# Kernel optimization log

Hardware: AMD Instinct MI355X
Metric: run time of the kernel (lower is better)

The kernel has to match this reference:

```python
import jax, jax.numpy as jnp
import numpy as np

HEADS = 16
HEAD_DIM = 64
DIM = 1024
INNER = HEADS * HEAD_DIM
EPS = 1e-5


def setup_inputs() -> dict:
    key = jax.random.key(0)
    ks = jax.random.split(key, 7)
    s_qkv = (2.0 / (DIM + 3 * INNER)) ** 0.5
    s_out = (2.0 / (INNER + DIM)) ** 0.5
    return {
        "x": jax.random.normal(ks[0], (4, 2048, DIM), dtype=jnp.float32),
        "w_qkv": jax.random.normal(ks[1], (DIM, 3 * INNER), dtype=jnp.float32) * s_qkv,
        "b_qkv": jnp.zeros((3 * INNER,), dtype=jnp.float32),
        "w_out": jax.random.normal(ks[2], (INNER, DIM), dtype=jnp.float32) * s_out,
        "b_out": jnp.zeros((DIM,), dtype=jnp.float32),
        "ln_gamma": jnp.ones((DIM,), dtype=jnp.float32),
        "ln_beta": jnp.zeros((DIM,), dtype=jnp.float32),
    }


def reference(x, w_qkv, b_qkv, w_out, b_out, ln_gamma, ln_beta):
    # Pre-norm LayerNorm
    mu = jnp.mean(x, axis=-1, keepdims=True)
    var = jnp.var(x, axis=-1, keepdims=True)
    xn = (x - mu) * jax.lax.rsqrt(var + EPS) * ln_gamma + ln_beta
    # QKV projection: [b, l, 3*inner]
    qkv = xn @ w_qkv + b_qkv
    q, k, v = jnp.split(qkv, 3, axis=-1)
    b, l, _ = x.shape
    def heads(t):  # [b, l, inner] -> [b, h, l, d]
        return t.reshape(b, l, HEADS, HEAD_DIM).transpose(0, 2, 1, 3)
    q, k, v = heads(q), heads(k), heads(v)
    scale = HEAD_DIM ** -0.5
    scores = jnp.einsum('bhqd,bhkd->bhqk', q, k) * scale
    att = jax.nn.softmax(scores, axis=-1)
    out = jnp.einsum('bhqk,bhkd->bhqd', att, v)
    out = out.transpose(0, 2, 1, 3).reshape(b, l, INNER)
    return out @ w_out + b_out
```

## Files before the change

### kernel.cpp

```cpp
#include <hip/hip_runtime.h>
#include <stdint.h>

typedef __bf16 bf16;
typedef bf16 bf16x4 __attribute__((ext_vector_type(4)));
typedef bf16 bf16x8 __attribute__((ext_vector_type(8)));
typedef float f32x4 __attribute__((ext_vector_type(4)));


__device__ __forceinline__ void gll16(const bf16* g, const bf16* l) {
  __builtin_amdgcn_global_load_lds(
      (__attribute__((address_space(1))) void*)(g),
      (__attribute__((address_space(3))) void*)(l),
      16, 0, 0);
}

__global__ __launch_bounds__(256) void ln_kernel(
    const float* __restrict__ x, const float* __restrict__ gamma,
    const float* __restrict__ beta, bf16* __restrict__ xn)
{
  __shared__ float red[8];
  const long row = blockIdx.x;
  const int t = threadIdx.x;
  f32x4 f = *(const f32x4*)(x + row * 1024 + t * 4);
  float sum = f[0] + f[1] + f[2] + f[3];
  float sq  = f[0]*f[0] + f[1]*f[1] + f[2]*f[2] + f[3]*f[3];
#pragma unroll
  for (int sh = 1; sh < 64; sh <<= 1) {
    sum += __shfl_xor(sum, sh, 64);
    sq  += __shfl_xor(sq,  sh, 64);
  }
  const int wave = t >> 6, lane = t & 63;
  if (lane == 0) { red[wave] = sum; red[wave + 4] = sq; }
  __syncthreads();
  sum = red[0] + red[1] + red[2] + red[3];
  sq  = red[4] + red[5] + red[6] + red[7];
  const float mu  = sum * (1.0f / 1024.0f);
  const float var = sq * (1.0f / 1024.0f) - mu * mu;
  const float rs  = rsqrtf(var + 1e-5f);
  f32x4 g = *(const f32x4*)(gamma + t * 4);
  f32x4 bb = *(const f32x4*)(beta + t * 4);
  bf16x4 ov;
#pragma unroll
  for (int i = 0; i < 4; i++)
    ov[i] = (bf16)((f[i] - mu) * rs * g[i] + bb[i]);
  *(bf16x4*)(xn + row * 1024 + t * 4) = ov;
}

__global__ __launch_bounds__(256) void transpose2_kernel(
    const float* __restrict__ wqkv, bf16* __restrict__ wqkvT,
    const float* __restrict__ wout, bf16* __restrict__ woutT)
{
  __shared__ bf16 tile[32][33];
  const int bx = blockIdx.x;
  const float* in;
  bf16* out;
  int Cc, c0;
  if (bx < 96) { in = wqkv; out = wqkvT; Cc = 3072; c0 = bx * 32; }
  else         { in = wout; out = woutT; Cc = 1024; c0 = (bx - 96) * 32; }
  const int r0 = blockIdx.y * 32;
  const int tx = threadIdx.x & 31, ty = threadIdx.x >> 5;
#pragma unroll
  for (int i = 0; i < 32; i += 8)
    tile[ty + i][tx] = (bf16)in[(long)(r0 + ty + i) * Cc + c0 + tx];
  __syncthreads();
#pragma unroll
  for (int i = 0; i < 32; i += 8)
    out[(long)(c0 + ty + i) * 1024 + r0 + tx] = tile[tx][ty + i];
}

__global__ __launch_bounds__(256, 2) void gemm_bt(
    const bf16* __restrict__ A, const bf16* __restrict__ BT,
    const float* __restrict__ bias, float* __restrict__ C,
    bf16* __restrict__ qb, bf16* __restrict__ kb, bf16* __restrict__ vtb,
    int K, int N, int mode)
{
  __shared__ bf16 sA[2][128 * 32];
  __shared__ bf16 sB[2][128 * 32];
  const int t = threadIdx.x;
  const int lane = t & 63;
  const int wave = t >> 6;
  const int wave_u = __builtin_amdgcn_readfirstlane(wave);
  const int quad = lane >> 4;
  const int c16 = lane & 15;
  const int wm = (wave >> 1) * 64;
  const int wn = (wave & 1) * 64;
  const int m0 = blockIdx.x * 128;
  const int n0 = blockIdx.y * 128;

  f32x4 acc[4][4] = {};

  const int srow = t >> 2;
  const int scol = (t & 3) * 8;
  const bf16* gA = A + (long)(m0 + srow) * K + scol;
  const bf16* gB = BT + (long)(n0 + srow) * K + scol;
  const bf16* lA = sA[0] + wave_u * 512;
  const bf16* lB = sB[0] + wave_u * 512;
  const long rowskip = (long)64 * K;

  gll16(gA, lA);
  gll16(gA + rowskip, lA + 2048);
  gll16(gB, lB);
  gll16(gB + rowskip, lB + 2048);

  int cur = 0;
  for (int k0 = 0; k0 < K; k0 += 32) {
    __syncthreads();
    const int kn = k0 + 32;
    if (kn < K) {
      const int alt = cur ^ 1;
      gll16(gA + kn, lA + alt * 4096);
      gll16(gA + kn + rowskip, lA + alt * 4096 + 2048);
      gll16(gB + kn, lB + alt * 4096);
      gll16(gB + kn + rowskip, lB + alt * 4096 + 2048);
    }
    const bf16* cA = sA[0] + cur * 4096;
    const bf16* cB = sB[0] + cur * 4096;
    bf16x8 af[4], bfr[4];
#pragma unroll
    for (int i = 0; i < 4; i++)
      af[i] = *(const bf16x8*)(cA + (wm + i * 16 + c16) * 32 + quad * 8);
#pragma unroll
    for (int j = 0; j < 4; j++)
      bfr[j] = *(const bf16x8*)(cB + (wn + j * 16 + c16) * 32 + quad * 8);
#pragma unroll
    for (int i = 0; i < 4; i++)
#pragma unroll
      for (int j = 0; j < 4; j++)
        acc[i][j] = __builtin_amdgcn_mfma_f32_16x16x32_bf16(af[i], bfr[j], acc[i][j], 0, 0, 0);
    cur ^= 1;
  }

#pragma unroll
  for (int i = 0; i < 4; i++) {
    const int mbase = m0 + wm + i * 16 + quad * 4;
#pragma unroll
    for (int j = 0; j < 4; j++) {
      const int n = n0 + wn + j * 16 + c16;
      const float bv = bias[n];
      if (mode == 0) {
#pragma unroll
        for (int r = 0; r < 4; r++)
          C[(long)(mbase + r) * N + n] = acc[i][j][r] + bv;
      } else {
        const int part = n >> 10;
        const int inner = n & 1023;
        const int h = inner >> 6, d = inner & 63;
#pragma unroll
        for (int r = 0; r < 4; r++) {
          const int m = mbase + r;
          const int b = m >> 11, l = m & 2047;
          const long bh = (long)((b << 4) | h);
          const float v = acc[i][j][r] + bv;
          if (part == 0)      qb [(bh * 2048 + l) * 64 + d] = (bf16)(v * 0.18033688f);
          else if (part == 1) kb [(bh * 2048 + l) * 64 + d] = (bf16)v;
          else                vtb[(bh * 64 + d) * 2048 + l] = (bf16)v;
        }
      }
    }
  }
}

__global__ __launch_bounds__(256, 4) void attn_kernel(
    const bf16* __restrict__ q, const bf16* __restrict__ k,
    const bf16* __restrict__ vt, bf16* __restrict__ att)
{
  __shared__ bf16 sK[128 * 68];
  __shared__ bf16 sVt[64 * 132];

  const int i = blockIdx.x;
  const int xcd = i & 7;
  const int wi = i >> 3;
  const int qt = wi & 15;
  const int bh = xcd * 8 + (wi >> 4);
  const int b = bh >> 4, h = bh & 15;
  const int q0 = qt * 128;
  const int t = threadIdx.x;
  const int wave = t >> 6, lane = t & 63;
  const int quad = lane >> 4, c16 = lane & 15;

  const bf16* qp = q + (long)bh * (2048 * 64);
  const bf16* kp = k + (long)bh * (2048 * 64);
  const bf16* vp = vt + (long)bh * (64 * 2048);

  bf16x8 aq[2][2];
#pragma unroll
  for (int m = 0; m < 2; m++) {
    const bf16* qrow = qp + (long)(q0 + wave * 32 + m * 16 + c16) * 64 + quad * 8;
    aq[m][0] = *(const bf16x8*)(qrow);
    aq[m][1] = *(const bf16x8*)(qrow + 32);
  }

  float p_sum[2] = {0.0f, 0.0f};
  f32x4 o_acc[2][4] = {};

  const int kr = t >> 3;
  const int kd = (t & 7) * 8;
  const int vr = t >> 4;
  const int vc = t & 15;
  const int vl = vc * 8;
  const int vD0 = (vc >> 2) * 32 + (vc & 1) * 16 + ((vc >> 1) & 1) * 4;

  bf16x8 kreg[4], vreg[4];
#pragma unroll
  for (int it = 0; it < 4; it++) {
    kreg[it] = *(const bf16x8*)(kp + (long)(it * 32 + kr) * 64 + kd);
    vreg[it] = *(const bf16x8*)(vp + (long)(it * 16 + vr) * 2048 + vl);
  }

  for (int kt = 0; kt < 16; kt++) {
    __syncthreads();
#pragma unroll
    for (int it = 0; it < 4; it++)
      *(bf16x8*)&sK[(it * 32 + kr) * 68 + kd] = kreg[it];
#pragma unroll
    for (int it = 0; it < 4; it++) {
      const bf16x8 v = vreg[it];
      const bf16x4 lo = __builtin_shufflevector(v, v, 0, 1, 2, 3);
      const bf16x4 hi = __builtin_shufflevector(v, v, 4, 5, 6, 7);
      bf16* d = &sVt[(it * 16 + vr) * 132 + vD0];
      *(bf16x4*)(d)     = lo;
      *(bf16x4*)(d + 8) = hi;
    }
    __syncthreads();

    const int kvn = ((kt + 1) & 15) * 128;

#pragma unroll
    for (int ks = 0; ks < 4; ks++) {
      bf16x8 ap[2];
#pragma unroll
      for (int e = 0; e < 2; e++) {
        const int jb = ks * 2 + e;
        const bf16x8 bk0 = *(const bf16x8*)&sK[(jb * 16 + c16) * 68 + quad * 8];
        const bf16x8 bk1 = *(const bf16x8*)&sK[(jb * 16 + c16) * 68 + 32 + quad * 8];
#pragma unroll
        for (int m = 0; m < 2; m++) {
          f32x4 z = {};
          z = __builtin_amdgcn_mfma_f32_16x16x32_bf16(bk0, aq[m][0], z, 0, 0, 0);
          z = __builtin_amdgcn_mfma_f32_16x16x32_bf16(bk1, aq[m][1], z, 0, 0, 0);
#pragma unroll
          for (int r = 0; r < 4; r++) {
            const float p = __builtin_amdgcn_exp2f(z[r]);
            p_sum[m] += p;
            ap[m][e * 4 + r] = (bf16)p;
          }
        }
      }
      if (ks == 1) {
#pragma unroll
        for (int it = 0; it < 4; it++)
          kreg[it] = *(const bf16x8*)(kp + (long)(kvn + it * 32 + kr) * 64 + kd);
      }
      if (ks == 2) {
#pragma unroll
        for (int it = 0; it < 4; it++)
          vreg[it] = *(const bf16x8*)(vp + (long)(it * 16 + vr) * 2048 + kvn + vl);
      }
#pragma unroll
      for (int jd = 0; jd < 4; jd++) {
        const bf16x8 bv = *(const bf16x8*)&sVt[(jd * 16 + c16) * 132 + ks * 32 + quad * 8];
        o_acc[0][jd] = __builtin_amdgcn_mfma_f32_16x16x32_bf16(ap[0], bv, o_acc[0][jd], 0, 0, 0);
        o_acc[1][jd] = __builtin_amdgcn_mfma_f32_16x16x32_bf16(ap[1], bv, o_acc[1][jd], 0, 0, 0);
      }
    }
  }

#pragma unroll
  for (int m = 0; m < 2; m++) {
    p_sum[m] += __shfl_xor(p_sum[m], 16, 64);
    p_sum[m] += __shfl_xor(p_sum[m], 32, 64);
  }

#pragma unroll
  for (int m = 0; m < 2; m++) {
#pragma unroll
    for (int r = 0; r < 4; r++) {
      const float ps = __shfl(p_sum[m], quad * 4 + r, 64);
      const float inv = 1.0f / ps;
      const long rowbase = ((long)b * 2048 + q0 + wave * 32 + m * 16 + quad * 4 + r) * 1024 + h * 64;
#pragma unroll
      for (int jd = 0; jd < 4; jd++)
        att[rowbase + jd * 16 + c16] = (bf16)(o_acc[m][jd][r] * inv);
    }
  }
}

extern "C" void kernel_launch(void* const* d_in, const int* in_sizes, int n_in,
                              void* d_out, int out_size, void* d_ws, size_t ws_size,
                              hipStream_t stream) {
  (void)in_sizes; (void)n_in; (void)out_size; (void)ws_size;
  const float* x     = (const float*)d_in[0];
  const float* w_qkv = (const float*)d_in[1];
  const float* b_qkv = (const float*)d_in[2];
  const float* w_out = (const float*)d_in[3];
  const float* b_out = (const float*)d_in[4];
  const float* gamma = (const float*)d_in[5];
  const float* beta  = (const float*)d_in[6];
  float* out = (float*)d_out;
  bf16* ws  = (bf16*)d_ws;

  bf16* xn    = ws;
  bf16* wqkvT = ws + 8388608;
  bf16* woutT = wqkvT + 3145728;
  bf16* qbuf  = woutT + 1048576;
  bf16* kbuf  = qbuf + 8388608;
  bf16* vtbuf = kbuf + 8388608;
  bf16* att   = xn;

  transpose2_kernel<<<dim3(128, 32), 256, 0, stream>>>(w_qkv, wqkvT, w_out, woutT);
  ln_kernel<<<dim3(8192), 256, 0, stream>>>(x, gamma, beta, xn);
  gemm_bt<<<dim3(8192 / 128, 3072 / 128), 256, 0, stream>>>(
      xn, wqkvT, b_qkv, (float*)nullptr, qbuf, kbuf, vtbuf, 1024, 3072, 1);
  attn_kernel<<<dim3(1024), 256, 0, stream>>>(qbuf, kbuf, vtbuf, att);
  gemm_bt<<<dim3(8192 / 128, 1024 / 128), 256, 0, stream>>>(
      att, woutT, b_out, out, (bf16*)nullptr, (bf16*)nullptr, (bf16*)nullptr, 1024, 1024, 0);
}
```

Baseline: 279.4 us.

## Triple-buffer GEMM LDS loads with explicit vmcnt waits and XOR swizzle

The bf16 GEMM goes from double- to triple-buffered LDS staging. Tiles are issued two k-steps ahead, and explicit s_waitcnt vmcnt counts plus raw s_barrier replace the per-iteration __syncthreads. The LDS layout gets an XOR swizzle on the 16-byte k-chunks, applied consistently on the global-load side and the fragment-read side, to cut bank conflicts. Launch bounds now target 3 blocks per CU, which raises LDS use to 48KB per block and may squeeze registers.

After: 283.9 us. Within noise of the previous version (+1.6%).

```diff
diff --git a/kernel.cpp b/kernel.cpp
--- a/kernel.cpp
+++ b/kernel.cpp
@@ -68,14 +68,14 @@
     out[(long)(c0 + ty + i) * 1024 + r0 + tx] = tile[tx][ty + i];
 }
 
-__global__ __launch_bounds__(256, 2) void gemm_bt(
+__global__ __launch_bounds__(256, 3) void gemm_bt(
     const bf16* __restrict__ A, const bf16* __restrict__ BT,
     const float* __restrict__ bias, float* __restrict__ C,
     bf16* __restrict__ qb, bf16* __restrict__ kb, bf16* __restrict__ vtb,
     int K, int N, int mode)
 {
-  __shared__ bf16 sA[2][128 * 32];
-  __shared__ bf16 sB[2][128 * 32];
+  __shared__ bf16 sA[3][128 * 32];
+  __shared__ bf16 sB[3][128 * 32];
   const int t = threadIdx.x;
   const int lane = t & 63;
   const int wave = t >> 6;
@@ -90,44 +90,57 @@
   f32x4 acc[4][4] = {};
 
   const int srow = t >> 2;
-  const int scol = (t & 3) * 8;
+  const int scol = (((t & 3) ^ ((t >> 3) & 3)) * 8);
   const bf16* gA = A + (long)(m0 + srow) * K + scol;
   const bf16* gB = BT + (long)(n0 + srow) * K + scol;
-  const bf16* lA = sA[0] + wave_u * 512;
-  const bf16* lB = sB[0] + wave_u * 512;
   const long rowskip = (long)64 * K;
-
-  gll16(gA, lA);
-  gll16(gA + rowskip, lA + 2048);
-  gll16(gB, lB);
-  gll16(gB + rowskip, lB + 2048);
-
-  int cur = 0;
-  for (int k0 = 0; k0 < K; k0 += 32) {
-    __syncthreads();
-    const int kn = k0 + 32;
-    if (kn < K) {
-      const int alt = cur ^ 1;
-      gll16(gA + kn, lA + alt * 4096);
-      gll16(gA + kn + rowskip, lA + alt * 4096 + 2048);
-      gll16(gB + kn, lB + alt * 4096);
-      gll16(gB + kn + rowskip, lB + alt * 4096 + 2048);
-    }
-    const bf16* cA = sA[0] + cur * 4096;
-    const bf16* cB = sB[0] + cur * 4096;
+  const int ksw = (quad ^ ((c16 >> 1) & 3)) * 8;
+
+  const int S = K >> 5;
+
+  auto stage = [&](int b, int kk) {
+    const bf16* lA = sA[0] + b * 4096 + wave_u * 512;
+    const bf16* lB = sB[0] + b * 4096 + wave_u * 512;
+    const int k0 = kk * 32;
+    gll16(gA + k0, lA);
+    gll16(gA + k0 + rowskip, lA + 2048);
+    gll16(gB + k0, lB);
+    gll16(gB + k0 + rowskip, lB + 2048);
+  };
+
+  stage(0, 0);
+  stage(1, 1);
+
+  int bcur = 0;
+  for (int s = 0; s < S; s++) {
+    if (s + 2 < S) {
+      const int bnx = (bcur >= 1) ? bcur - 1 : 2;
+      stage(bnx, s + 2);
+      asm volatile("s_waitcnt vmcnt(8)" ::: "memory");
+    } else if (s + 1 < S) {
+      asm volatile("s_waitcnt vmcnt(4)" ::: "memory");
+    } else {
+      asm volatile("s_waitcnt vmcnt(0)" ::: "memory");
+    }
+    __builtin_amdgcn_s_barrier();
+
+    const bf16* cA = sA[0] + bcur * 4096;
+    const bf16* cB = sB[0] + bcur * 4096;
     bf16x8 af[4], bfr[4];
 #pragma unroll
     for (int i = 0; i < 4; i++)
-      af[i] = *(const bf16x8*)(cA + (wm + i * 16 + c16) * 32 + quad * 8);
+      af[i] = *(const bf16x8*)(cA + (wm + i * 16 + c16) * 32 + ksw);
 #pragma unroll
     for (int j = 0; j < 4; j++)
-      bfr[j] = *(const bf16x8*)(cB + (wn + j * 16 + c16) * 32 + quad * 8);
+      bfr[j] = *(const bf16x8*)(cB + (wn + j * 16 + c16) * 32 + ksw);
 #pragma unroll
     for (int i = 0; i < 4; i++)
 #pragma unroll
       for (int j = 0; j < 4; j++)
         acc[i][j] = __builtin_amdgcn_mfma_f32_16x16x32_bf16(af[i], bfr[j], acc[i][j], 0, 0, 0);
-    cur ^= 1;
+
+    __builtin_amdgcn_s_barrier();
+    bcur = (bcur == 2) ? 0 : bcur + 1;
   }
 
 #pragma unroll
```
